# Optimization experiments

Hardware: AMD Instinct MI355X
Metric: run time of the kernel (lower is better)

Reference implementation:

```python
import jax, jax.numpy as jnp
import numpy as np

BS = 16384   # batch size
D = 2048     # input_dim
BD = 64      # block_dim
NB = D // BD # 32 blocks per BlockMLP
H = 2 * BD   # hidden block dim (hidden_layers_ratio=[2])
NUM_LAYERS = 2  # ceil(log_64(2048)) = 2


def setup_inputs() -> dict:
    key = jax.random.key(0)
    ks = jax.random.split(key, 1 + 2 * NUM_LAYERS)
    inp = {"x": jax.random.normal(ks[0], (BS, D), dtype=jnp.float32)}
    for i in range(NUM_LAYERS):
        inp[f"W1_{i}"] = jax.random.normal(ks[1 + 2 * i], (NB, BD, H), dtype=jnp.float32)
        inp[f"b1_{i}"] = jnp.zeros((NB, 1, H), dtype=jnp.float32)
        inp[f"W2_{i}"] = jax.random.normal(ks[2 + 2 * i], (NB, H, BD), dtype=jnp.float32)
        inp[f"b2_{i}"] = jnp.zeros((NB, 1, BD), dtype=jnp.float32)
    return inp


def _block_mlp(y, W1, b1, W2, b2):
    # BlockMLP.forward: view(bs, n_blocks, block_dim) -> transpose to [n_blocks, bs, block_dim]
    bs = y.shape[0]
    yb = y.reshape(bs, NB, BD).transpose(1, 0, 2)          # [NB, bs, BD]
    h = jnp.einsum('nbi,nio->nbo', yb, W1) + b1             # [NB, bs, H]
    h = jax.nn.gelu(h, approximate=False)                   # torch nn.GELU default (erf)
    o = jnp.einsum('nbh,nho->nbo', h, W2) + b2              # [NB, bs, BD]
    return o.transpose(1, 0, 2).reshape(bs, -1)             # [bs, D]


def reference(x, W1_0, b1_0, W2_0, b2_0, W1_1, b1_1, W2_1, b2_1):
    bs = x.shape[0]
    params = [(W1_0, b1_0, W2_0, b2_0), (W1_1, b1_1, W2_1, b2_1)]
    y = x
    for i, (W1, b1, W2, b2) in enumerate(params):
        # butterfly-style mixing permute before the block MLP
        y = y.reshape(-1, BD, BD ** i).transpose(0, 2, 1).reshape(bs, -1)
        y = _block_mlp(y, W1, b1, W2, b2)
        # inverse-style permute after
        y = y.reshape(-1, BD ** i, BD).transpose(0, 2, 1)
    return y.reshape(bs, -1)
```

## Files before the change

kernel.cpp:

```cpp
#include <hip/hip_runtime.h>

#define D    2048
#define NB   32
#define BD   64
#define HD   128
#define WSZ  (NB * HD * BD)
#define TSZ  (16384 * 64)

typedef __attribute__((ext_vector_type(8))) short short8;
typedef __attribute__((ext_vector_type(4))) float floatx4;

static __device__ __forceinline__ unsigned short f2bf(float f) {
  union { float f; unsigned u; } v; v.f = f;
  return (unsigned short)((v.u + 0x7FFFu + ((v.u >> 16) & 1u)) >> 16);
}
static __device__ __forceinline__ float bf2f(unsigned short h) {
  union { unsigned u; float f; } v; v.u = ((unsigned)h) << 16;
  return v.f;
}
static __device__ __forceinline__ unsigned fbits(float f) {
  union { float f; unsigned u; } v; v.f = f; return v.u;
}
static __device__ __forceinline__ unsigned short tbf(float f) {
  return (unsigned short)(fbits(f) >> 16);
}
static __device__ __forceinline__ unsigned pkt(float a, float b) {
  return __builtin_amdgcn_perm(fbits(b), fbits(a), 0x07060302u);
}
static __device__ __forceinline__ float fast_exp2(float x) {
  float r; asm("v_exp_f32 %0, %1" : "=v"(r) : "v"(x)); return r;
}
static __device__ __forceinline__ float fast_rcp(float x) {
  float r; asm("v_rcp_f32 %0, %1" : "=v"(r) : "v"(x)); return r;
}
static __device__ __forceinline__ float gelu_f(float x) {
  float x2 = x * x;
  float w  = __builtin_fmaf(x2, -0.102943695f, -2.3022083f);
  float e  = fast_exp2(x * w);
  return x * fast_rcp(1.0f + e);
}

__global__ __launch_bounds__(256, 3) void mlp0_k(
    const float* __restrict__ xf,
    unsigned short* __restrict__ Yt0,
    const unsigned short* __restrict__ Wt1,
    const unsigned short* __restrict__ Wt2,
    const float* __restrict__ b1, const float* __restrict__ b2) {
  __shared__ unsigned short Wlds[16384];
  __shared__ unsigned short Olds[64 * 128];
  __shared__ float Blds[192];
  const int n     = blockIdx.x & 31;
  const int chunk = blockIdx.x >> 5;
  const int t = threadIdx.x, l = t & 63, wv = t >> 6;
  const int lr = l & 15, q = l >> 4;
  const int sw = (lr & 7) << 3;
  const int rbase = chunk * 128 + wv * 32 + lr;

  const unsigned short* s1 = Wt1 + n * 8192;
  const unsigned short* s2 = Wt2 + n * 8192;
  short8 sv1[4], sv2[4];
#pragma unroll
  for (int j = 0; j < 4; ++j) {
    sv1[j] = *(const short8*)&s1[(j * 256 + t) * 8];
    sv2[j] = *(const short8*)&s2[(j * 256 + t) * 8];
  }
  float bv = 0.f;
  if (t < 128)      bv = b1[n * HD + t];
  else if (t < 192) bv = b2[n * BD + (t - 128)];
  float4 uf[2][4];
#pragma unroll
  for (int p = 0; p < 2; ++p) {
    const float* xr = xf + (size_t)(rbase + p * 16) * D + n * BD + q * 8;
    uf[p][0] = *(const float4*)(xr);      uf[p][1] = *(const float4*)(xr + 4);
    uf[p][2] = *(const float4*)(xr + 32); uf[p][3] = *(const float4*)(xr + 36);
  }
  asm volatile("" ::: "memory");
#pragma unroll
  for (int j = 0; j < 4; ++j) {
    *(short8*)&Wlds[(j * 256 + t) * 8]        = sv1[j];
    *(short8*)&Wlds[8192 + (j * 256 + t) * 8] = sv2[j];
  }
  if (t < 192) Blds[t] = bv;
  __syncthreads();

  const unsigned short* w1p0 = &Wlds[lr * 64 + ((q * 8) ^ sw)];
  const unsigned short* w1p1 = &Wlds[lr * 64 + ((32 + q * 8) ^ sw)];
  const unsigned short* w2p0 = &Wlds[8192 + lr * 128 + ((q * 8) ^ sw)];
  const unsigned short* w2p1 = &Wlds[8192 + lr * 128 + ((32 + q * 8) ^ sw)];

#pragma unroll
  for (int i = 0; i < 2; ++i) {
    short8 xb0, xb1;
    {
      union { unsigned u[4]; short8 s; } c0, c1;
      c0.u[0] = pkt(uf[i][0].x, uf[i][0].y);
      c0.u[1] = pkt(uf[i][0].z, uf[i][0].w);
      c0.u[2] = pkt(uf[i][1].x, uf[i][1].y);
      c0.u[3] = pkt(uf[i][1].z, uf[i][1].w);
      c1.u[0] = pkt(uf[i][2].x, uf[i][2].y);
      c1.u[1] = pkt(uf[i][2].z, uf[i][2].w);
      c1.u[2] = pkt(uf[i][3].x, uf[i][3].y);
      c1.u[3] = pkt(uf[i][3].z, uf[i][3].w);
      xb0 = c0.s; xb1 = c1.s;
    }
    floatx4 acc2[4];
#pragma unroll
    for (int ot = 0; ot < 4; ++ot) {
      const float4 bb = *(const float4*)&Blds[128 + ot * 16 + q * 4];
      floatx4 v; v[0] = bb.x; v[1] = bb.y; v[2] = bb.z; v[3] = bb.w;
      acc2[ot] = v;
    }
#pragma unroll
    for (int hf = 0; hf < 2; ++hf) {
      floatx4 acc1[4];
#pragma unroll
      for (int ot = 0; ot < 4; ++ot) {
        const float4 bb = *(const float4*)&Blds[hf * 64 + ot * 16 + q * 4];
        floatx4 v; v[0] = bb.x; v[1] = bb.y; v[2] = bb.z; v[3] = bb.w;
        acc1[ot] = v;
      }
#pragma unroll
      for (int ot = 0; ot < 4; ++ot) {
        const int off = (hf * 64 + ot * 16) * 64;
        short8 a0 = *(const short8*)&w1p0[off];
        short8 a1 = *(const short8*)&w1p1[off];
        acc1[ot] = __builtin_amdgcn_mfma_f32_16x16x32_bf16(a0, xb0, acc1[ot], 0, 0, 0);
        acc1[ot] = __builtin_amdgcn_mfma_f32_16x16x32_bf16(a1, xb1, acc1[ot], 0, 0, 0);
      }
      union { unsigned u[4]; short8 s; } hb0, hb1;
      hb0.u[0] = pkt(gelu_f(acc1[0][0]), gelu_f(acc1[0][1]));
      hb0.u[1] = pkt(gelu_f(acc1[0][2]), gelu_f(acc1[0][3]));
      hb0.u[2] = pkt(gelu_f(acc1[1][0]), gelu_f(acc1[1][1]));
      hb0.u[3] = pkt(gelu_f(acc1[1][2]), gelu_f(acc1[1][3]));
      hb1.u[0] = pkt(gelu_f(acc1[2][0]), gelu_f(acc1[2][1]));
      hb1.u[1] = pkt(gelu_f(acc1[2][2]), gelu_f(acc1[2][3]));
      hb1.u[2] = pkt(gelu_f(acc1[3][0]), gelu_f(acc1[3][1]));
      hb1.u[3] = pkt(gelu_f(acc1[3][2]), gelu_f(acc1[3][3]));
#pragma unroll
      for (int ot = 0; ot < 4; ++ot) {
        const int off = ot * 16 * 128 + hf * 64;
        short8 w0 = *(const short8*)&w2p0[off];
        short8 w1 = *(const short8*)&w2p1[off];
        acc2[ot] = __builtin_amdgcn_mfma_f32_16x16x32_bf16(w0, hb0.s, acc2[ot], 0, 0, 0);
        acc2[ot] = __builtin_amdgcn_mfma_f32_16x16x32_bf16(w1, hb1.s, acc2[ot], 0, 0, 0);
      }
    }
    const int rl = wv * 32 + i * 16 + lr;
#pragma unroll
    for (int ot = 0; ot < 4; ++ot) {
#pragma unroll
      for (int e = 0; e < 4; ++e) {
        const int fo = ot * 16 + q * 4 + e;
        Olds[fo * 128 + (rl ^ ((fo & 7) << 3))] = tbf(acc2[ot][e]);
      }
    }
  }
  __syncthreads();

  const int j = t & 63, w = t >> 6;
#pragma unroll
  for (int ii = 0; ii < 8; ++ii) {
    const int fo = w * 16 + ii * 2 + (j >> 5);
    const int r4 = (j & 31) * 4;
    const int G  = (fo & 7) << 3;
    uint2 v = *(const uint2*)&Olds[fo * 128 + (r4 ^ G)];
    *(uint2*)(Yt0 + (size_t)n * TSZ + (size_t)fo * 16384 + chunk * 128 + r4) = v;
  }
}

__global__ __launch_bounds__(256, 3) void mlp1_k(
    const unsigned short* __restrict__ Yt0,
    unsigned short* __restrict__ Yt1,
    const unsigned short* __restrict__ Wt1,
    const unsigned short* __restrict__ Wt2,
    const float* __restrict__ b1, const float* __restrict__ b2) {
  __shared__ unsigned short Wlds[16384];
  __shared__ unsigned short Xl[2 * 128 * 32];
  __shared__ float Blds[192];
  const int np    = blockIdx.x & 31;
  const int chunk = blockIdx.x >> 5;
  const int t = threadIdx.x, l = t & 63, wv = t >> 6;
  const int lr = l & 15, q = l >> 4;
  const int sw = (lr & 7) << 3;

  const unsigned short* s1 = Wt1 + np * 8192;
  const unsigned short* s2 = Wt2 + np * 8192;
  short8 sv1[4], sv2[4];
#pragma unroll
  for (int j = 0; j < 4; ++j) {
    sv1[j] = *(const short8*)&s1[(j * 256 + t) * 8];
    sv2[j] = *(const short8*)&s2[(j * 256 + t) * 8];
  }
  float bv = 0.f;
  if (t < 128)      bv = b1[np * HD + t];
  else if (t < 192) bv = b2[np * BD + (t - 128)];
  const int c = t >> 2, sub = t & 3;
  const int sp = c >> 5, sn = c & 31;
  const unsigned short* src = Yt0 + (size_t)sn * TSZ + (size_t)(sp * 32 + np) * 16384
                              + chunk * 128 + sub * 32;
  short8 sx[4];
#pragma unroll
  for (int m = 0; m < 4; ++m) sx[m] = *(const short8*)(src + m * 8);

  asm volatile("" ::: "memory");
#pragma unroll
  for (int j = 0; j < 4; ++j) {
    *(short8*)&Wlds[(j * 256 + t) * 8]        = sv1[j];
    *(short8*)&Wlds[8192 + (j * 256 + t) * 8] = sv2[j];
  }
  if (t < 192) Blds[t] = bv;
#pragma unroll
  for (int m = 0; m < 4; ++m) {
#pragma unroll
    for (int k = 0; k < 8; ++k) {
      const int row = sub * 32 + m * 8 + k;
      Xl[sp * 4096 + row * 32 + (sn ^ (((row >> 1) & 3) << 3))] = (unsigned short)sx[m][k];
    }
  }
  __syncthreads();

  const unsigned short* w1p0 = &Wlds[lr * 64 + ((q * 8) ^ sw)];
  const unsigned short* w1p1 = &Wlds[lr * 64 + ((32 + q * 8) ^ sw)];
  const unsigned short* w2p0 = &Wlds[8192 + lr * 128 + ((q * 8) ^ sw)];
  const unsigned short* w2p1 = &Wlds[8192 + lr * 128 + ((32 + q * 8) ^ sw)];
  const int p = lr & 1;

#pragma unroll
  for (int i = 0; i < 2; ++i) {
    const int rloc = (wv * 32 + i * 16 + lr) & ~1;
    const int g0   = ((rloc >> 1) & 3) << 3;
    short8 xb0 = *(const short8*)&Xl[p * 4096 + rloc * 32 + ((q * 8) ^ g0)];
    short8 xb1 = *(const short8*)&Xl[p * 4096 + (rloc + 1) * 32 + ((q * 8) ^ g0)];

    floatx4 acc2[4];
#pragma unroll
    for (int ot = 0; ot < 4; ++ot) {
      const float4 bb = *(const float4*)&Blds[128 + ot * 16 + q * 4];
      floatx4 v; v[0] = bb.x; v[1] = bb.y; v[2] = bb.z; v[3] = bb.w;
      acc2[ot] = v;
    }
#pragma unroll
    for (int hf = 0; hf < 2; ++hf) {
      floatx4 acc1[4];
#pragma unroll
      for (int ot = 0; ot < 4; ++ot) {
        const float4 bb = *(const float4*)&Blds[hf * 64 + ot * 16 + q * 4];
        floatx4 v; v[0] = bb.x; v[1] = bb.y; v[2] = bb.z; v[3] = bb.w;
        acc1[ot] = v;
      }
#pragma unroll
      for (int ot = 0; ot < 4; ++ot) {
        const int off = (hf * 64 + ot * 16) * 64;
        short8 a0 = *(const short8*)&w1p0[off];
        short8 a1 = *(const short8*)&w1p1[off];
        acc1[ot] = __builtin_amdgcn_mfma_f32_16x16x32_bf16(a0, xb0, acc1[ot], 0, 0, 0);
        acc1[ot] = __builtin_amdgcn_mfma_f32_16x16x32_bf16(a1, xb1, acc1[ot], 0, 0, 0);
      }
      union { unsigned u[4]; short8 s; } hb0, hb1;
      hb0.u[0] = pkt(gelu_f(acc1[0][0]), gelu_f(acc1[0][1]));
      hb0.u[1] = pkt(gelu_f(acc1[0][2]), gelu_f(acc1[0][3]));
      hb0.u[2] = pkt(gelu_f(acc1[1][0]), gelu_f(acc1[1][1]));
      hb0.u[3] = pkt(gelu_f(acc1[1][2]), gelu_f(acc1[1][3]));
      hb1.u[0] = pkt(gelu_f(acc1[2][0]), gelu_f(acc1[2][1]));
      hb1.u[1] = pkt(gelu_f(acc1[2][2]), gelu_f(acc1[2][3]));
      hb1.u[2] = pkt(gelu_f(acc1[3][0]), gelu_f(acc1[3][1]));
      hb1.u[3] = pkt(gelu_f(acc1[3][2]), gelu_f(acc1[3][3]));
#pragma unroll
      for (int ot = 0; ot < 4; ++ot) {
        const int off = ot * 16 * 128 + hf * 64;
        short8 w0 = *(const short8*)&w2p0[off];
        short8 w1 = *(const short8*)&w2p1[off];
        acc2[ot] = __builtin_amdgcn_mfma_f32_16x16x32_bf16(w0, hb0.s, acc2[ot], 0, 0, 0);
        acc2[ot] = __builtin_amdgcn_mfma_f32_16x16x32_bf16(w1, hb1.s, acc2[ot], 0, 0, 0);
      }
    }
    unsigned short* yo = Yt1 + (size_t)np * TSZ
                       + (size_t)(chunk * 128 + wv * 32 + i * 16 + lr) * 64;
#pragma unroll
    for (int ot = 0; ot < 4; ++ot) {
      ushort4 ov;
      ov.x = f2bf(acc2[ot][0]);
      ov.y = f2bf(acc2[ot][1]);
      ov.z = f2bf(acc2[ot][2]);
      ov.w = f2bf(acc2[ot][3]);
      *(ushort4*)&yo[ot * 16 + q * 4] = ov;
    }
  }
}

__global__ __launch_bounds__(256) void unpermute_k(const unsigned short* __restrict__ Y,
                                                   float* __restrict__ out) {
  __shared__ unsigned short L[32 * 512];
  const int t = threadIdx.x, w = t >> 6, j = t & 63;
  const size_t r0 = (size_t)blockIdx.x * 8;
#pragma unroll
  for (int c = 0; c < 8; ++c) {
    const int n = w * 8 + c;
    short8 v = *(const short8*)(Y + (size_t)n * TSZ + r0 * 64 + j * 8);
    const int row = j >> 3;
    const int gp = (j & 7) ^ ((n + row) & 7);
    *(short8*)&L[n * 512 + row * 64 + gp * 8] = v;
  }
  __syncthreads();
#pragma unroll
  for (int p = 0; p < 2; ++p) {
    const int rloc = w * 2 + p;
    float* op = out + (r0 + rloc) * (size_t)D;
#pragma unroll
    for (int i = 0; i < 8; ++i) {
      const int cbase = i * 256 + j * 4;
      float4 f;
#pragma unroll
      for (int e = 0; e < 4; ++e) {
        const int cc   = cbase + e;
        const int npp  = cc >> 6, fp = cc & 63;
        const int n    = fp & 31;
        const int srow = (rloc & ~1) | (fp >> 5);
        const int scol = (rloc & 1) * 32 + npp;
        const int g    = ((scol >> 3) ^ ((n + srow) & 7));
        const float v  = bf2f(L[n * 512 + srow * 64 + g * 8 + (scol & 7)]);
        if      (e == 0) f.x = v;
        else if (e == 1) f.y = v;
        else if (e == 2) f.z = v;
        else             f.w = v;
      }
      *(float4*)&op[cbase] = f;
    }
  }
}

__global__ void prep_w_all(const float* __restrict__ W1_0, const float* __restrict__ W2_0,
                           const float* __restrict__ W1_1, const float* __restrict__ W2_1,
                           unsigned short* __restrict__ dst) {
  const int seg = blockIdx.x >> 10;
  const int id  = ((blockIdx.x & 1023) << 8) | threadIdx.x;
  const float* W; int R;
  if      (seg == 0) { W = W1_0; R = BD; }
  else if (seg == 1) { W = W2_0; R = HD; }
  else if (seg == 2) { W = W1_1; R = BD; }
  else               { W = W2_1; R = HD; }
  const int C   = (R == BD) ? HD : BD;
  const int n   = id >> 13;
  const int rem = id & 8191;
  const int c   = rem / R;
  const int r   = rem - c * R;
  const unsigned short val = f2bf(W[(n * R + r) * C + c]);
  if (seg & 1) {
    const int hf  = r >> 6, st = (r >> 5) & 1, blk = (r >> 4) & 1;
    const int qq  = (r & 15) >> 2, e = r & 3;
    const int slot = hf * 64 + st * 32 + qq * 8 + blk * 4 + e;
    dst[seg * WSZ + n * 8192 + c * HD + (slot ^ ((c & 7) << 3))] = val;
  } else {
    dst[seg * WSZ + n * 8192 + c * BD + (r ^ ((c & 7) << 3))] = val;
  }
}

extern "C" void kernel_launch(void* const* d_in, const int* in_sizes, int n_in,
                              void* d_out, int out_size, void* d_ws, size_t ws_size,
                              hipStream_t stream) {
  const float* x    = (const float*)d_in[0];
  const float* W1_0 = (const float*)d_in[1];
  const float* b1_0 = (const float*)d_in[2];
  const float* W2_0 = (const float*)d_in[3];
  const float* b2_0 = (const float*)d_in[4];
  const float* W1_1 = (const float*)d_in[5];
  const float* b1_1 = (const float*)d_in[6];
  const float* W2_1 = (const float*)d_in[7];
  const float* b2_1 = (const float*)d_in[8];
  float* out = (float*)d_out;

  unsigned short* Wt  = (unsigned short*)d_ws;
  unsigned short* Yt0 = Wt + 4 * WSZ;
  unsigned short* Yt1 = Yt0 + (size_t)NB * TSZ;

  prep_w_all<<<4096, 256, 0, stream>>>(W1_0, W2_0, W1_1, W2_1, Wt);
  mlp0_k<<<4096, 256, 0, stream>>>(x, Yt0, Wt, Wt + WSZ, b1_0, b2_0);
  mlp1_k<<<4096, 256, 0, stream>>>(Yt0, Yt1, Wt + 2 * WSZ, Wt + 3 * WSZ, b1_1, b2_1);
  unpermute_k<<<2048, 256, 0, stream>>>(Yt1, out);
}
```

Baseline: 140.6 us.

## Process two row chunks per block with prefetch of next chunk's inputs

Both MLP kernels now handle 256 rows per block instead of 128, which halves the grid and amortizes the per-block weight load into LDS over twice the work. The global loads for the second half's input are issued before the first half's MFMA compute runs, so their latency overlaps with that compute. The cost is higher register pressure from the prefetch buffers, extra __syncthreads, and fewer blocks available to fill the GPU.

Result: no change. 141.2 us (+0.4%).

```diff
diff --git a/kernel.cpp b/kernel.cpp
--- a/kernel.cpp
+++ b/kernel.cpp
@@ -54,7 +54,7 @@
   const int t = threadIdx.x, l = t & 63, wv = t >> 6;
   const int lr = l & 15, q = l >> 4;
   const int sw = (lr & 7) << 3;
-  const int rbase = chunk * 128 + wv * 32 + lr;
+  const size_t rowbase = (size_t)chunk * 256;
 
   const unsigned short* s1 = Wt1 + n * 8192;
   const unsigned short* s2 = Wt2 + n * 8192;
@@ -70,7 +70,7 @@
   float4 uf[2][4];
 #pragma unroll
   for (int p = 0; p < 2; ++p) {
-    const float* xr = xf + (size_t)(rbase + p * 16) * D + n * BD + q * 8;
+    const float* xr = xf + (rowbase + p * 64 + wv * 16 + lr) * D + n * BD + q * 8;
     uf[p][0] = *(const float4*)(xr);      uf[p][1] = *(const float4*)(xr + 4);
     uf[p][2] = *(const float4*)(xr + 32); uf[p][3] = *(const float4*)(xr + 36);
   }
@@ -89,82 +89,94 @@
   const unsigned short* w2p1 = &Wlds[8192 + lr * 128 + ((32 + q * 8) ^ sw)];
 
 #pragma unroll
-  for (int i = 0; i < 2; ++i) {
-    short8 xb0, xb1;
-    {
-      union { unsigned u[4]; short8 s; } c0, c1;
-      c0.u[0] = pkt(uf[i][0].x, uf[i][0].y);
-      c0.u[1] = pkt(uf[i][0].z, uf[i][0].w);
-      c0.u[2] = pkt(uf[i][1].x, uf[i][1].y);
-      c0.u[3] = pkt(uf[i][1].z, uf[i][1].w);
-      c1.u[0] = pkt(uf[i][2].x, uf[i][2].y);
-      c1.u[1] = pkt(uf[i][2].z, uf[i][2].w);
-      c1.u[2] = pkt(uf[i][3].x, uf[i][3].y);
-      c1.u[3] = pkt(uf[i][3].z, uf[i][3].w);
-      xb0 = c0.s; xb1 = c1.s;
-    }
-    floatx4 acc2[4];
-#pragma unroll
-    for (int ot = 0; ot < 4; ++ot) {
-      const float4 bb = *(const float4*)&Blds[128 + ot * 16 + q * 4];
-      floatx4 v; v[0] = bb.x; v[1] = bb.y; v[2] = bb.z; v[3] = bb.w;
-      acc2[ot] = v;
-    }
-#pragma unroll
-    for (int hf = 0; hf < 2; ++hf) {
-      floatx4 acc1[4];
+  for (int half = 0; half < 2; ++half) {
+#pragma unroll
+    for (int it = 0; it < 2; ++it) {
+      const int i    = half * 2 + it;
+      const int slot = i & 1;
+      short8 xb0, xb1;
+      {
+        union { unsigned u[4]; short8 s; } c0, c1;
+        c0.u[0] = pkt(uf[slot][0].x, uf[slot][0].y);
+        c0.u[1] = pkt(uf[slot][0].z, uf[slot][0].w);
+        c0.u[2] = pkt(uf[slot][1].x, uf[slot][1].y);
+        c0.u[3] = pkt(uf[slot][1].z, uf[slot][1].w);
+        c1.u[0] = pkt(uf[slot][2].x, uf[slot][2].y);
+        c1.u[1] = pkt(uf[slot][2].z, uf[slot][2].w);
+        c1.u[2] = pkt(uf[slot][3].x, uf[slot][3].y);
+        c1.u[3] = pkt(uf[slot][3].z, uf[slot][3].w);
+        xb0 = c0.s; xb1 = c1.s;
+      }
+      if (i < 2) {
+        const float* xr = xf + (rowbase + (i + 2) * 64 + wv * 16 + lr) * D + n * BD + q * 8;
+        uf[slot][0] = *(const float4*)(xr);      uf[slot][1] = *(const float4*)(xr + 4);
+        uf[slot][2] = *(const float4*)(xr + 32); uf[slot][3] = *(const float4*)(xr + 36);
+        asm volatile("" ::: "memory");
+      }
+
+      floatx4 acc2[4];
 #pragma unroll
       for (int ot = 0; ot < 4; ++ot) {
-        const float4 bb = *(const float4*)&Blds[hf * 64 + ot * 16 + q * 4];
+        const float4 bb = *(const float4*)&Blds[128 + ot * 16 + q * 4];
         floatx4 v; v[0] = bb.x; v[1] = bb.y; v[2] = bb.z; v[3] = bb.w;
-        acc1[ot] = v;
-      }
+        acc2[ot] = v;
+      }
+#pragma unroll
+      for (int hf = 0; hf < 2; ++hf) {
+        floatx4 acc1[4];
+#pragma unroll
+        for (int ot = 0; ot < 4; ++ot) {
+          const float4 bb = *(const float4*)&Blds[hf * 64 + ot * 16 + q * 4];
+          floatx4 v; v[0] = bb.x; v[1] = bb.y; v[2] = bb.z; v[3] = bb.w;
+          acc1[ot] = v;
+        }
+#pragma unroll
+        for (int ot = 0; ot < 4; ++ot) {
+          const int off = (hf * 64 + ot * 16) * 64;
+          short8 a0 = *(const short8*)&w1p0[off];
+          short8 a1 = *(const short8*)&w1p1[off];
+          acc1[ot] = __builtin_amdgcn_mfma_f32_16x16x32_bf16(a0, xb0, acc1[ot], 0, 0, 0);
+          acc1[ot] = __builtin_amdgcn_mfma_f32_16x16x32_bf16(a1, xb1, acc1[ot], 0, 0, 0);
+        }
+        union { unsigned u[4]; short8 s; } hb0, hb1;
+        hb0.u[0] = pkt(gelu_f(acc1[0][0]), gelu_f(acc1[0][1]));
+        hb0.u[1] = pkt(gelu_f(acc1[0][2]), gelu_f(acc1[0][3]));
+        hb0.u[2] = pkt(gelu_f(acc1[1][0]), gelu_f(acc1[1][1]));
+        hb0.u[3] = pkt(gelu_f(acc1[1][2]), gelu_f(acc1[1][3]));
+        hb1.u[0] = pkt(gelu_f(acc1[2][0]), gelu_f(acc1[2][1]));
+        hb1.u[1] = pkt(gelu_f(acc1[2][2]), gelu_f(acc1[2][3]));
+        hb1.u[2] = pkt(gelu_f(acc1[3][0]), gelu_f(acc1[3][1]));
+        hb1.u[3] = pkt(gelu_f(acc1[3][2]), gelu_f(acc1[3][3]));
+#pragma unroll
+        for (int ot = 0; ot < 4; ++ot) {
+          const int off = ot * 16 * 128 + hf * 64;
+          short8 w0 = *(const short8*)&w2p0[off];
+          short8 w1 = *(const short8*)&w2p1[off];
+          acc2[ot] = __builtin_amdgcn_mfma_f32_16x16x32_bf16(w0, hb0.s, acc2[ot], 0, 0, 0);
+          acc2[ot] = __builtin_amdgcn_mfma_f32_16x16x32_bf16(w1, hb1.s, acc2[ot], 0, 0, 0);
+        }
+      }
+      const int rl = it * 64 + wv * 16 + lr;
 #pragma unroll
       for (int ot = 0; ot < 4; ++ot) {
-        const int off = (hf * 64 + ot * 16) * 64;
-        short8 a0 = *(const short8*)&w1p0[off];
-        short8 a1 = *(const short8*)&w1p1[off];
-        acc1[ot] = __builtin_amdgcn_mfma_f32_16x16x32_bf16(a0, xb0, acc1[ot], 0, 0, 0);
-        acc1[ot] = __builtin_amdgcn_mfma_f32_16x16x32_bf16(a1, xb1, acc1[ot], 0, 0, 0);
-      }
-      union { unsigned u[4]; short8 s; } hb0, hb1;
-      hb0.u[0] = pkt(gelu_f(acc1[0][0]), gelu_f(acc1[0][1]));
-      hb0.u[1] = pkt(gelu_f(acc1[0][2]), gelu_f(acc1[0][3]));
-      hb0.u[2] = pkt(gelu_f(acc1[1][0]), gelu_f(acc1[1][1]));
-      hb0.u[3] = pkt(gelu_f(acc1[1][2]), gelu_f(acc1[1][3]));
-      hb1.u[0] = pkt(gelu_f(acc1[2][0]), gelu_f(acc1[2][1]));
-      hb1.u[1] = pkt(gelu_f(acc1[2][2]), gelu_f(acc1[2][3]));
-      hb1.u[2] = pkt(gelu_f(acc1[3][0]), gelu_f(acc1[3][1]));
-      hb1.u[3] = pkt(gelu_f(acc1[3][2]), gelu_f(acc1[3][3]));
-#pragma unroll
-      for (int ot = 0; ot < 4; ++ot) {
-        const int off = ot * 16 * 128 + hf * 64;
-        short8 w0 = *(const short8*)&w2p0[off];
-        short8 w1 = *(const short8*)&w2p1[off];
-        acc2[ot] = __builtin_amdgcn_mfma_f32_16x16x32_bf16(w0, hb0.s, acc2[ot], 0, 0, 0);
-        acc2[ot] = __builtin_amdgcn_mfma_f32_16x16x32_bf16(w1, hb1.s, acc2[ot], 0, 0, 0);
-      }
-    }
-    const int rl = wv * 32 + i * 16 + lr;
-#pragma unroll
-    for (int ot = 0; ot < 4; ++ot) {
-#pragma unroll
-      for (int e = 0; e < 4; ++e) {
-        const int fo = ot * 16 + q * 4 + e;
-        Olds[fo * 128 + (rl ^ ((fo & 7) << 3))] = tbf(acc2[ot][e]);
-      }
-    }
-  }
-  __syncthreads();
-
-  const int j = t & 63, w = t >> 6;
-#pragma unroll
-  for (int ii = 0; ii < 8; ++ii) {
-    const int fo = w * 16 + ii * 2 + (j >> 5);
-    const int r4 = (j & 31) * 4;
-    const int G  = (fo & 7) << 3;
-    uint2 v = *(const uint2*)&Olds[fo * 128 + (r4 ^ G)];
-    *(uint2*)(Yt0 + (size_t)n * TSZ + (size_t)fo * 16384 + chunk * 128 + r4) = v;
+#pragma unroll
+        for (int e = 0; e < 4; ++e) {
+          const int fo = ot * 16 + q * 4 + e;
+          Olds[fo * 128 + (rl ^ ((fo & 7) << 3))] = tbf(acc2[ot][e]);
+        }
+      }
+    }
+    __syncthreads();
+    const int j = t & 63, w = t >> 6;
+#pragma unroll
+    for (int ii = 0; ii < 8; ++ii) {
+      const int fo = w * 16 + ii * 2 + (j >> 5);
+      const int r4 = (j & 31) * 4;
+      const int G  = (fo & 7) << 3;
+      uint2 v = *(const uint2*)&Olds[fo * 128 + (r4 ^ G)];
+      *(uint2*)(Yt0 + (size_t)n * TSZ + (size_t)fo * 16384 + rowbase + half * 128 + r4) = v;
+    }
+    if (half == 0) __syncthreads();
   }
 }
 
@@ -182,6 +194,7 @@
   const int t = threadIdx.x, l = t & 63, wv = t >> 6;
   const int lr = l & 15, q = l >> 4;
   const int sw = (lr & 7) << 3;
+  const size_t rowbase = (size_t)chunk * 256;
 
   const unsigned short* s1 = Wt1 + np * 8192;
   const unsigned short* s2 = Wt2 + np * 8192;
@@ -196,11 +209,11 @@
   else if (t < 192) bv = b2[np * BD + (t - 128)];
   const int c = t >> 2, sub = t & 3;
   const int sp = c >> 5, sn = c & 31;
-  const unsigned short* src = Yt0 + (size_t)sn * TSZ + (size_t)(sp * 32 + np) * 16384
-                              + chunk * 128 + sub * 32;
+  const unsigned short* src0 = Yt0 + (size_t)sn * TSZ + (size_t)(sp * 32 + np) * 16384
+                               + rowbase + sub * 32;
   short8 sx[4];
 #pragma unroll
-  for (int m = 0; m < 4; ++m) sx[m] = *(const short8*)(src + m * 8);
+  for (int m = 0; m < 4; ++m) sx[m] = *(const short8*)(src0 + m * 8);
 
   asm volatile("" ::: "memory");
 #pragma unroll
@@ -226,64 +239,86 @@
   const int p = lr & 1;
 
 #pragma unroll
-  for (int i = 0; i < 2; ++i) {
-    const int rloc = (wv * 32 + i * 16 + lr) & ~1;
-    const int g0   = ((rloc >> 1) & 3) << 3;
-    short8 xb0 = *(const short8*)&Xl[p * 4096 + rloc * 32 + ((q * 8) ^ g0)];
-    short8 xb1 = *(const short8*)&Xl[p * 4096 + (rloc + 1) * 32 + ((q * 8) ^ g0)];
-
-    floatx4 acc2[4];
-#pragma unroll
-    for (int ot = 0; ot < 4; ++ot) {
-      const float4 bb = *(const float4*)&Blds[128 + ot * 16 + q * 4];
-      floatx4 v; v[0] = bb.x; v[1] = bb.y; v[2] = bb.z; v[3] = bb.w;
-      acc2[ot] = v;
-    }
-#pragma unroll
-    for (int hf = 0; hf < 2; ++hf) {
-      floatx4 acc1[4];
+  for (int half = 0; half < 2; ++half) {
+    short8 sx2[4];
+    if (half == 0) {
+      const unsigned short* src1 = src0 + 128;
+#pragma unroll
+      for (int m = 0; m < 4; ++m) sx2[m] = *(const short8*)(src1 + m * 8);
+      asm volatile("" ::: "memory");
+    }
+#pragma unroll
+    for (int i = 0; i < 2; ++i) {
+      const int rloc = (wv * 32 + i * 16 + lr) & ~1;
+      const int g0   = ((rloc >> 1) & 3) << 3;
+      short8 xb0 = *(const short8*)&Xl[p * 4096 + rloc * 32 + ((q * 8) ^ g0)];
+      short8 xb1 = *(const short8*)&Xl[p * 4096 + (rloc + 1) * 32 + ((q * 8) ^ g0)];
+
+      floatx4 acc2[4];
 #pragma unroll
       for (int ot = 0; ot < 4; ++ot) {
-        const float4 bb = *(const float4*)&Blds[hf * 64 + ot * 16 + q * 4];
+        const float4 bb = *(const float4*)&Blds[128 + ot * 16 + q * 4];
         floatx4 v; v[0] = bb.x; v[1] = bb.y; v[2] = bb.z; v[3] = bb.w;
-        acc1[ot] = v;
-      }
+        acc2[ot] = v;
+      }
+#pragma unroll
+      for (int hf = 0; hf < 2; ++hf) {
+        floatx4 acc1[4];
+#pragma unroll
+        for (int ot = 0; ot < 4; ++ot) {
+          const float4 bb = *(const float4*)&Blds[hf * 64 + ot * 16 + q * 4];
+          floatx4 v; v[0] = bb.x; v[1] = bb.y; v[2] = bb.z; v[3] = bb.w;
+          acc1[ot] = v;
+        }
+#pragma unroll
+        for (int ot = 0; ot < 4; ++ot) {
+          const int off = (hf * 64 + ot * 16) * 64;
+          short8 a0 = *(const short8*)&w1p0[off];
+          short8 a1 = *(const short8*)&w1p1[off];
+          acc1[ot] = __builtin_amdgcn_mfma_f32_16x16x32_bf16(a0, xb0, acc1[ot], 0, 0, 0);
+          acc1[ot] = __builtin_amdgcn_mfma_f32_16x16x32_bf16(a1, xb1, acc1[ot], 0, 0, 0);
+        }
+        union { unsigned u[4]; short8 s; } hb0, hb1;
+        hb0.u[0] = pkt(gelu_f(acc1[0][0]), gelu_f(acc1[0][1]));
+        hb0.u[1] = pkt(gelu_f(acc1[0][2]), gelu_f(acc1[0][3]));
+        hb0.u[2] = pkt(gelu_f(acc1[1][0]), gelu_f(acc1[1][1]));
+        hb0.u[3] = pkt(gelu_f(acc1[1][2]), gelu_f(acc1[1][3]));
+        hb1.u[0] = pkt(gelu_f(acc1[2][0]), gelu_f(acc1[2][1]));
+        hb1.u[1] = pkt(gelu_f(acc1[2][2]), gelu_f(acc1[2][3]));
+        hb1.u[2] = pkt(gelu_f(acc1[3][0]), gelu_f(acc1[3][1]));
+        hb1.u[3] = pkt(gelu_f(acc1[3][2]), gelu_f(acc1[3][3]));
+#pragma unroll
+        for (int ot = 0; ot < 4; ++ot) {
+          const int off = ot * 16 * 128 + hf * 64;
+          short8 w0 = *(const short8*)&w2p0[off];
+          short8 w1 = *(const short8*)&w2p1[off];
+          acc2[ot] = __builtin_amdgcn_mfma_f32_16x16x32_bf16(w0, hb0.s, acc2[ot], 0, 0, 0);
+          acc2[ot] = __builtin_amdgcn_mfma_f32_16x16x32_bf16(w1, hb1.s, acc2[ot], 0, 0, 0);
+        }
+      }
+      unsigned short* yo = Yt1 + (size_t)np * TSZ
+                         + (rowbase + half * 128 + wv * 32 + i * 16 + lr) * 64;
 #pragma unroll
       for (int ot = 0; ot < 4; ++ot) {
-        const int off = (hf * 64 + ot * 16) * 64;
-        short8 a0 = *(const short8*)&w1p0[off];
-        short8 a1 = *(const short8*)&w1p1[off];
-        acc1[ot] = __builtin_amdgcn_mfma_f32_16x16x32_bf16(a0, xb0, acc1[ot], 0, 0, 0);
-        acc1[ot] = __builtin_amdgcn_mfma_f32_16x16x32_bf16(a1, xb1, acc1[ot], 0, 0, 0);
-      }
-      union { unsigned u[4]; short8 s; } hb0, hb1;
-      hb0.u[0] = pkt(gelu_f(acc1[0][0]), gelu_f(acc1[0][1]));
-      hb0.u[1] = pkt(gelu_f(acc1[0][2]), gelu_f(acc1[0][3]));
-      hb0.u[2] = pkt(gelu_f(acc1[1][0]), gelu_f(acc1[1][1]));
-      hb0.u[3] = pkt(gelu_f(acc1[1][2]), gelu_f(acc1[1][3]));
-      hb1.u[0] = pkt(gelu_f(acc1[2][0]), gelu_f(acc1[2][1]));
-      hb1.u[1] = pkt(gelu_f(acc1[2][2]), gelu_f(acc1[2][3]));
-      hb1.u[2] = pkt(gelu_f(acc1[3][0]), gelu_f(acc1[3][1]));
-      hb1.u[3] = pkt(gelu_f(acc1[3][2]), gelu_f(acc1[3][3]));
-#pragma unroll
-      for (int ot = 0; ot < 4; ++ot) {
-        const int off = ot * 16 * 128 + hf * 64;
-        short8 w0 = *(const short8*)&w2p0[off];
-        short8 w1 = *(const short8*)&w2p1[off];
-        acc2[ot] = __builtin_amdgcn_mfma_f32_16x16x32_bf16(w0, hb0.s, acc2[ot], 0, 0, 0);
-        acc2[ot] = __builtin_amdgcn_mfma_f32_16x16x32_bf16(w1, hb1.s, acc2[ot], 0, 0, 0);
-      }
-    }
-    unsigned short* yo = Yt1 + (size_t)np * TSZ
-                       + (size_t)(chunk * 128 + wv * 32 + i * 16 + lr) * 64;
-#pragma unroll
-    for (int ot = 0; ot < 4; ++ot) {
-      ushort4 ov;
-      ov.x = f2bf(acc2[ot][0]);
-      ov.y = f2bf(acc2[ot][1]);
-      ov.z = f2bf(acc2[ot][2]);
-      ov.w = f2bf(acc2[ot][3]);
-      *(ushort4*)&yo[ot * 16 + q * 4] = ov;
+        ushort4 ov;
+        ov.x = f2bf(acc2[ot][0]);
+        ov.y = f2bf(acc2[ot][1]);
+        ov.z = f2bf(acc2[ot][2]);
+        ov.w = f2bf(acc2[ot][3]);
+        *(ushort4*)&yo[ot * 16 + q * 4] = ov;
+      }
+    }
+    if (half == 0) {
+      __syncthreads();
+#pragma unroll
+      for (int m = 0; m < 4; ++m) {
+#pragma unroll
+        for (int k = 0; k < 8; ++k) {
+          const int row = sub * 32 + m * 8 + k;
+          Xl[sp * 4096 + row * 32 + (sn ^ (((row >> 1) & 3) << 3))] = (unsigned short)sx2[m][k];
+        }
+      }
+      __syncthreads();
     }
   }
 }
@@ -374,7 +409,7 @@
   unsigned short* Yt1 = Yt0 + (size_t)NB * TSZ;
 
   prep_w_all<<<4096, 256, 0, stream>>>(W1_0, W2_0, W1_1, W2_1, Wt);
-  mlp0_k<<<4096, 256, 0, stream>>>(x, Yt0, Wt, Wt + WSZ, b1_0, b2_0);
-  mlp1_k<<<4096, 256, 0, stream>>>(Yt0, Yt1, Wt + 2 * WSZ, Wt + 3 * WSZ, b1_1, b2_1);
+  mlp0_k<<<2048, 256, 0, stream>>>(x, Yt0, Wt, Wt + WSZ, b1_0, b2_0);
+  mlp1_k<<<2048, 256, 0, stream>>>(Yt0, Yt1, Wt + 2 * WSZ, Wt + 3 * WSZ, b1_1, b2_1);
   unpermute_k<<<2048, 256, 0, stream>>>(Yt1, out);
 }
```
